# Kernel optimization log

Hardware: AMD Instinct MI355X
Metric: run time of the kernel (lower is better)

## Reference

```python
import jax, jax.numpy as jnp
import numpy as np

E = 8        # num experts
TOP = 2      # top-k
D = 1024     # emb_size


def setup_inputs() -> dict:
    key = jax.random.key(0)
    ks = jax.random.split(key, 8)
    s = 1.0 / np.sqrt(D)
    x = jax.random.normal(ks[0], (4, 2048, D), dtype=jnp.float32)
    Wg = jax.random.uniform(ks[1], (D, E), jnp.float32, -s, s)
    bg = jax.random.uniform(ks[2], (E,), jnp.float32, -s, s)
    W1 = jax.random.uniform(ks[3], (E, D, D), jnp.float32, -s, s)
    b1 = jax.random.uniform(ks[4], (E, D), jnp.float32, -s, s)
    W2 = jax.random.uniform(ks[5], (E, D, D), jnp.float32, -s, s)
    b2 = jax.random.uniform(ks[6], (E, D), jnp.float32, -s, s)
    return {"x": x, "Wg": Wg, "bg": bg, "W1": W1, "b1": b1, "W2": W2, "b2": b2}


def reference(x, Wg, bg, W1, b1, W2, b2):
    x_shape = x.shape
    xt = x.reshape(-1, x_shape[-1])                       # [N, D] tokens
    gate_prob = jax.nn.softmax(xt @ Wg + bg, axis=-1)     # [N, E]
    top_w, top_i = jax.lax.top_k(gate_prob, TOP)          # [N, TOP]
    top_w = jax.nn.softmax(top_w, axis=-1)                # renormalize over top-k
    N = xt.shape[0]
    # combine weights scattered into dense [N, E] (each token has TOP nonzeros)
    comb = jnp.zeros((N, E), xt.dtype).at[jnp.arange(N)[:, None], top_i].add(top_w)
    # per-expert 2-layer MLP applied to all tokens; masked-out tokens get 0 combine weight
    h = jax.nn.relu(jnp.einsum('nd,edf->enf', xt, W1) + b1[:, None, :])   # [E, N, D]
    ye = jnp.einsum('enf,efg->eng', h, W2) + b2[:, None, :]               # [E, N, D]
    y = jnp.einsum('ne,eng->ng', comb, ye)                                # [N, D]
    return y.reshape(x_shape), gate_prob
```

## Files before the change

### kernel.cpp

```cpp
#include <hip/hip_runtime.h>
#include <stdint.h>

#define TOKENS 8192
#define DIM    1024
#define NEXP   8
#define NASSIGN (TOKENS*2)
#define BK     64

#define C_ROW   16
#define C_TILE  25
#define C_TOTAL 34

#define WS_CTRL  0
#define WS_TOPE  1024
#define WS_TOPW  (WS_TOPE + NASSIGN*4)
#define WS_PTOK  (WS_TOPW + NASSIGN*4)
#define WS_PW    (WS_PTOK + NASSIGN*4)
#define WS_XB    (WS_PW  + NASSIGN*4)
#define WS_W1T   (WS_XB  + (size_t)TOKENS*DIM*2)
#define WS_W2T   (WS_W1T + (size_t)NEXP*DIM*DIM*2)
#define WS_H     (WS_W2T + (size_t)NEXP*DIM*DIM*2)

#define WGLD (DIM + 4)

typedef __attribute__((ext_vector_type(8))) short short8;
typedef __attribute__((ext_vector_type(4))) float floatx4;

__device__ __forceinline__ uint32_t bfr(float f) {
  uint32_t v = __float_as_uint(f);
  return (v + 0x7FFFu + ((v >> 16) & 1u)) >> 16;
}
__device__ __forceinline__ float b2f(uint32_t u) { return __uint_as_float(u << 16); }

__device__ __forceinline__ void load_lds16(const void* g, void* l) {
  __builtin_amdgcn_global_load_lds(
      (const __attribute__((address_space(1))) uint32_t*)g,
      (__attribute__((address_space(3))) uint32_t*)l, 16, 0, 0);
}

__global__ __launch_bounds__(256) void gate_kernel(
    const float* __restrict__ x, const float* __restrict__ Wg,
    const float* __restrict__ bg, float* __restrict__ gate_out,
    int* __restrict__ top_e, float* __restrict__ top_w,
    uint16_t* __restrict__ xb, float* __restrict__ y) {
  __shared__ __align__(16) float wgs[NEXP * WGLD];
  int t = threadIdx.x;

  {
    float4 z = make_float4(0.f, 0.f, 0.f, 0.f);
    float4* yz = (float4*)(y + (size_t)blockIdx.x * 4 * DIM);
    #pragma unroll
    for (int i = 0; i < 4; i++) yz[i * 256 + t] = z;
  }

  #pragma unroll
  for (int k = 0; k < 32; k++) {
    int i = k * 256 + t;
    float v = Wg[i];
    wgs[(i & 7) * WGLD + (i >> 3)] = v;
  }
  __syncthreads();

  int wave = t >> 6, lane = t & 63;
  int tok = blockIdx.x * 4 + wave;
  const float4* xr = (const float4*)(x + (size_t)tok * DIM);
  uint2* xw = (uint2*)(xb + (size_t)tok * DIM);

  float4 acc[NEXP];
  #pragma unroll
  for (int e = 0; e < NEXP; e++) acc[e] = make_float4(0.f, 0.f, 0.f, 0.f);

  #pragma unroll
  for (int c = 0; c < 4; c++) {
    float4 xv = xr[c * 64 + lane];
    uint2 o;
    o.x = bfr(xv.x) | (bfr(xv.y) << 16);
    o.y = bfr(xv.z) | (bfr(xv.w) << 16);
    xw[c * 64 + lane] = o;
    int d0 = (c * 64 + lane) * 4;
    #pragma unroll
    for (int e = 0; e < NEXP; e++) {
      float4 wv = *(const float4*)&wgs[e * WGLD + d0];
      acc[e].x = fmaf(xv.x, wv.x, acc[e].x);
      acc[e].y = fmaf(xv.y, wv.y, acc[e].y);
      acc[e].z = fmaf(xv.z, wv.z, acc[e].z);
      acc[e].w = fmaf(xv.w, wv.w, acc[e].w);
    }
  }
  float s[NEXP];
  #pragma unroll
  for (int e = 0; e < NEXP; e++) s[e] = (acc[e].x + acc[e].y) + (acc[e].z + acc[e].w);
  #pragma unroll
  for (int off = 32; off > 0; off >>= 1) {
    #pragma unroll
    for (int e = 0; e < NEXP; e++) s[e] += __shfl_xor(s[e], off);
  }
  if (lane == 0) {
    float lg[NEXP], p[NEXP];
    float mx = -1e30f;
    #pragma unroll
    for (int e = 0; e < NEXP; e++) { lg[e] = s[e] + bg[e]; mx = fmaxf(mx, lg[e]); }
    float sum = 0.f;
    #pragma unroll
    for (int e = 0; e < NEXP; e++) { p[e] = expf(lg[e] - mx); sum += p[e]; }
    float inv = 1.f / sum;
    #pragma unroll
    for (int e = 0; e < NEXP; e++) p[e] *= inv;
    float4* go = (float4*)(gate_out + (size_t)tok * NEXP);
    go[0] = make_float4(p[0], p[1], p[2], p[3]);
    go[1] = make_float4(p[4], p[5], p[6], p[7]);
    int i1 = 0;
    #pragma unroll
    for (int e = 1; e < NEXP; e++) if (p[e] > p[i1]) i1 = e;
    int i2 = (i1 == 0) ? 1 : 0;
    #pragma unroll
    for (int e = 0; e < NEXP; e++) if (e != i1 && p[e] > p[i2]) i2 = e;
    float ev = expf(p[i2] - p[i1]);
    float w1 = 1.f / (1.f + ev), w2 = ev / (1.f + ev);
    top_e[2*tok]   = i1; top_e[2*tok+1] = i2;
    top_w[2*tok]   = w1; top_w[2*tok+1] = w2;
  }
}

__global__ __launch_bounds__(256) void prep2_kernel(
    const float* __restrict__ W1, const float* __restrict__ W2,
    uint16_t* __restrict__ W1T, uint16_t* __restrict__ W2T,
    const int* __restrict__ top_e, const float* __restrict__ top_w,
    int* __restrict__ ctrl, int* __restrict__ ptok, float* __restrict__ pw) {
  __shared__ __align__(16) char smem[64 * 68 * 2];
  __shared__ int scnt[NEXP];
  __shared__ int rowstart[NEXP];
  int t = threadIdx.x;

  if (blockIdx.x != 0) {
    uint16_t (*tile)[68] = (uint16_t (*)[68])smem;
    int cb = blockIdx.x - 1;
    int m  = cb >> 8;
    int d0 = ((cb >> 4) & 15) * 64, f0 = (cb & 15) * 64;
    const float* src = (m < 8) ? (W1 + (size_t)m*DIM*DIM) : (W2 + (size_t)(m-8)*DIM*DIM);
    uint16_t*    dst = (m < 8) ? (W1T + (size_t)m*DIM*DIM) : (W2T + (size_t)(m-8)*DIM*DIM);
    int col = t & 63, rb = (t >> 6) * 16;
    #pragma unroll
    for (int i = 0; i < 16; i++) {
      int dr = rb + i;
      tile[dr][col] = (uint16_t)bfr(src[(size_t)(d0+dr)*DIM + f0 + col]);
    }
    __syncthreads();
    int dg = t & 15, frb = t >> 4;
    #pragma unroll
    for (int i = 0; i < 4; i++) {
      int fr = frb + i * 16;
      uint32_t b0 = tile[dg*4+0][fr], b1 = tile[dg*4+1][fr];
      uint32_t b2 = tile[dg*4+2][fr], b3 = tile[dg*4+3][fr];
      uint2 v;
      v.x = b0 | (b1 << 16);
      v.y = b2 | (b3 << 16);
      *(uint2*)&dst[(size_t)(f0+fr)*DIM + d0 + dg*4] = v;
    }
    return;
  }

  int* sc = (int*)smem;
  int cnt[NEXP];
  #pragma unroll
  for (int e = 0; e < NEXP; e++) cnt[e] = 0;
  for (int j = 0; j < 64; j++) {
    int e = top_e[t * 64 + j];
    cnt[e]++;
  }
  #pragma unroll
  for (int e = 0; e < NEXP; e++) sc[e * 256 + t] = cnt[e];
  __syncthreads();
  int wave = t >> 6, lane = t & 63;
  for (int ee = wave; ee < NEXP; ee += 4) {
    int running = 0;
    for (int chunk = 0; chunk < 4; chunk++) {
      int idx = ee * 256 + chunk * 64 + lane;
      int v = sc[idx];
      int incl = v;
      #pragma unroll
      for (int off = 1; off < 64; off <<= 1) {
        int u = __shfl_up(incl, off);
        if (lane >= off) incl += u;
      }
      sc[idx] = running + incl - v;
      running += __shfl(incl, 63);
    }
    if (lane == 0) scnt[ee] = running;
  }
  __syncthreads();
  if (t == 0) {
    int rs = 0, ts = 0;
    for (int e = 0; e < NEXP; e++) {
      ctrl[C_ROW + e] = rs;
      ctrl[C_TILE + e] = ts;
      rowstart[e] = rs;
      int c = scnt[e];
      rs += c;
      ts += (c + 127) >> 7;
    }
    ctrl[C_ROW + NEXP] = rs;
    ctrl[C_TILE + NEXP] = ts;
    ctrl[C_TOTAL] = ts;
  }
  __syncthreads();
  int off[NEXP];
  #pragma unroll
  for (int e = 0; e < NEXP; e++) off[e] = rowstart[e] + sc[e * 256 + t];
  for (int j = 0; j < 64; j++) {
    int i = t * 64 + j;
    int e = top_e[i];
    int pos = off[e]++;
    ptok[pos] = i >> 1;
    pw[pos]   = top_w[i];
  }
}

__device__ __forceinline__ bool sched_map(const int* ctrl, int bid,
                                          int& mtile, int& n0) {
  int total = ctrl[C_TOTAL];
  int spx = (total + 7) >> 3;
  int xcd = bid & 7, j = bid >> 3;
  int slot = j >> 3;
  if (slot >= spx) return false;
  mtile = xcd * spx + slot;
  n0 = (j & 7) * 128;
  return mtile < total;
}

__global__ __launch_bounds__(256, 2) void gemm1_kernel(
    const uint16_t* __restrict__ xb, const uint16_t* __restrict__ w1t,
    const float* __restrict__ b1, const int* __restrict__ ctrl,
    const int* __restrict__ ptok, uint16_t* __restrict__ h) {
  __shared__ __align__(16) uint16_t As[128*BK];
  __shared__ __align__(16) uint16_t Bs[128*BK];
  int mtile, n0;
  if (!sched_map(ctrl, blockIdx.x, mtile, n0)) return;
  int e = 0;
  #pragma unroll
  for (int k = 1; k < NEXP; k++) if (mtile >= ctrl[C_TILE + k]) e = k;
  int row0 = ctrl[C_ROW + e] + (mtile - ctrl[C_TILE + e]) * 128;
  int rend = ctrl[C_ROW + e + 1];

  int t = threadIdx.x, lane = t & 63, w = t >> 6;
  const uint16_t* gA[4];
  const uint16_t* gB[4];
  #pragma unroll
  for (int i = 0; i < 4; i++) {
    int s = i * 256 + t;
    int row = s >> 3, cs = s & 7;
    int gc = cs ^ (row & 7);
    int ar = row0 + row; if (ar > NASSIGN-1) ar = NASSIGN-1;
    int tok = ptok[ar];
    gA[i] = xb  + (size_t)tok * DIM + gc*8;
    gB[i] = w1t + (size_t)e*DIM*DIM + (size_t)(n0 + row)*DIM + gc*8;
  }
  floatx4 acc[4][4];
  #pragma unroll
  for (int mi = 0; mi < 4; mi++)
    #pragma unroll
    for (int ni = 0; ni < 4; ni++) acc[mi][ni] = (floatx4)(0.f);

  int wm = w & 1, wn = w >> 1;
  int l15 = lane & 15, lq = lane >> 4;

  for (int kt = 0; kt < DIM/BK; kt++) {
    #pragma unroll
    for (int i = 0; i < 4; i++) {
      load_lds16(gA[i], &As[(i*256 + t) * 8]);
      load_lds16(gB[i], &Bs[(i*256 + t) * 8]);
      gA[i] += BK; gB[i] += BK;
    }
    __syncthreads();
    #pragma unroll
    for (int ks = 0; ks < 2; ks++) {
      short8 a[4], b[4];
      #pragma unroll
      for (int mi = 0; mi < 4; mi++) {
        int row = wm*64 + mi*16 + l15;
        int slot = (ks*4 + lq) ^ (row & 7);
        a[mi] = *(const short8*)&As[row*BK + slot*8];
      }
      #pragma unroll
      for (int ni = 0; ni < 4; ni++) {
        int row = wn*64 + ni*16 + l15;
        int slot = (ks*4 + lq) ^ (row & 7);
        b[ni] = *(const short8*)&Bs[row*BK + slot*8];
      }
      #pragma unroll
      for (int mi = 0; mi < 4; mi++)
        #pragma unroll
        for (int ni = 0; ni < 4; ni++)
          acc[mi][ni] = __builtin_amdgcn_mfma_f32_16x16x32_bf16(a[mi], b[ni], acc[mi][ni], 0, 0, 0);
    }
    __syncthreads();
  }
  #pragma unroll
  for (int mi = 0; mi < 4; mi++) {
    #pragma unroll
    for (int r = 0; r < 4; r++) {
      int rt = wm*64 + mi*16 + lq*4 + r;
      int ar = row0 + rt;
      if (ar < rend) {
        #pragma unroll
        for (int ni = 0; ni < 4; ni++) {
          int n = n0 + wn*64 + ni*16 + l15;
          float v = acc[mi][ni][r] + b1[e*DIM + n];
          v = fmaxf(v, 0.f);
          h[(size_t)ar*DIM + n] = (uint16_t)bfr(v);
        }
      }
    }
  }
}

__global__ __launch_bounds__(256, 2) void gemm2_kernel(
    const uint16_t* __restrict__ h, const uint16_t* __restrict__ w2t,
    const float* __restrict__ b2, const int* __restrict__ ctrl,
    const int* __restrict__ ptok, const float* __restrict__ pw,
    float* __restrict__ y) {
  __shared__ __align__(16) uint16_t As[128*BK];
  __shared__ __align__(16) uint16_t Bs[128*BK];
  int mtile, n0;
  if (!sched_map(ctrl, blockIdx.x, mtile, n0)) return;
  int e = 0;
  #pragma unroll
  for (int k = 1; k < NEXP; k++) if (mtile >= ctrl[C_TILE + k]) e = k;
  int row0 = ctrl[C_ROW + e] + (mtile - ctrl[C_TILE + e]) * 128;
  int rend = ctrl[C_ROW + e + 1];

  int t = threadIdx.x, lane = t & 63, w = t >> 6;
  const uint16_t* gA[4];
  const uint16_t* gB[4];
  #pragma unroll
  for (int i = 0; i < 4; i++) {
    int s = i * 256 + t;
    int row = s >> 3, cs = s & 7;
    int gc = cs ^ (row & 7);
    int ar = row0 + row; if (ar > NASSIGN-1) ar = NASSIGN-1;
    gA[i] = h   + (size_t)ar * DIM + gc*8;
    gB[i] = w2t + (size_t)e*DIM*DIM + (size_t)(n0 + row)*DIM + gc*8;
  }
  floatx4 acc[4][4];
  #pragma unroll
  for (int mi = 0; mi < 4; mi++)
    #pragma unroll
    for (int ni = 0; ni < 4; ni++) acc[mi][ni] = (floatx4)(0.f);

  int wm = w & 1, wn = w >> 1;
  int l15 = lane & 15, lq = lane >> 4;

  for (int kt = 0; kt < DIM/BK; kt++) {
    #pragma unroll
    for (int i = 0; i < 4; i++) {
      load_lds16(gA[i], &As[(i*256 + t) * 8]);
      load_lds16(gB[i], &Bs[(i*256 + t) * 8]);
      gA[i] += BK; gB[i] += BK;
    }
    __syncthreads();
    #pragma unroll
    for (int ks = 0; ks < 2; ks++) {
      short8 a[4], b[4];
      #pragma unroll
      for (int mi = 0; mi < 4; mi++) {
        int row = wm*64 + mi*16 + l15;
        int slot = (ks*4 + lq) ^ (row & 7);
        a[mi] = *(const short8*)&As[row*BK + slot*8];
      }
      #pragma unroll
      for (int ni = 0; ni < 4; ni++) {
        int row = wn*64 + ni*16 + l15;
        int slot = (ks*4 + lq) ^ (row & 7);
        b[ni] = *(const short8*)&Bs[row*BK + slot*8];
      }
      #pragma unroll
      for (int mi = 0; mi < 4; mi++)
        #pragma unroll
        for (int ni = 0; ni < 4; ni++)
          acc[mi][ni] = __builtin_amdgcn_mfma_f32_16x16x32_bf16(a[mi], b[ni], acc[mi][ni], 0, 0, 0);
    }
    __syncthreads();
  }
  #pragma unroll
  for (int mi = 0; mi < 4; mi++) {
    #pragma unroll
    for (int r = 0; r < 4; r++) {
      int rt = wm*64 + mi*16 + lq*4 + r;
      int ar = row0 + rt;
      if (ar < rend) {
        int tok   = ptok[ar];
        float wgt = pw[ar];
        float* yrow = y + (size_t)tok * DIM;
        #pragma unroll
        for (int ni = 0; ni < 4; ni++) {
          int n = n0 + wn*64 + ni*16 + l15;
          float v = acc[mi][ni][r] + b2[e*DIM + n];
          unsafeAtomicAdd(&yrow[n], wgt * v);
        }
      }
    }
  }
}

extern "C" void kernel_launch(void* const* d_in, const int* in_sizes, int n_in,
                              void* d_out, int out_size, void* d_ws, size_t ws_size,
                              hipStream_t stream) {
  const float* x  = (const float*)d_in[0];
  const float* Wg = (const float*)d_in[1];
  const float* bg = (const float*)d_in[2];
  const float* W1 = (const float*)d_in[3];
  const float* b1 = (const float*)d_in[4];
  const float* W2 = (const float*)d_in[5];
  const float* b2 = (const float*)d_in[6];
  float* out = (float*)d_out;
  char* ws = (char*)d_ws;

  int*      ctrl = (int*)(ws + WS_CTRL);
  int*      tope = (int*)(ws + WS_TOPE);
  float*    topw = (float*)(ws + WS_TOPW);
  int*      ptok = (int*)(ws + WS_PTOK);
  float*    pww  = (float*)(ws + WS_PW);
  uint16_t* xb   = (uint16_t*)(ws + WS_XB);
  uint16_t* w1t  = (uint16_t*)(ws + WS_W1T);
  uint16_t* w2t  = (uint16_t*)(ws + WS_W2T);
  uint16_t* hbuf = (uint16_t*)(ws + WS_H);

  gate_kernel<<<2048, 256, 0, stream>>>(x, Wg, bg, out + (size_t)TOKENS*DIM,
                                        tope, topw, xb, out);
  prep2_kernel<<<4097, 256, 0, stream>>>(W1, W2, w1t, w2t, tope, topw,
                                         ctrl, ptok, pww);
  gemm1_kernel<<<136*8, 256, 0, stream>>>(xb, w1t, b1, ctrl, ptok, hbuf);
  gemm2_kernel<<<136*8, 256, 0, stream>>>(hbuf, w2t, b2, ctrl, ptok, pww, out);
}
```

Measured before the change: 329.7 us.

## Replace atomic scatter-add in gemm2 with bf16 per-assignment output and combine kernel

gemm2 no longer does fp32 atomic adds into y. It writes each assignment's expert output as bf16 into a buffer that reuses the xb workspace, and a new combine kernel gathers each token's two rows and sums them with the top-k weights. This also removes the zero-fill of y from the gate kernel and the pw permutation, adding an arow inverse map instead. The goal is to avoid scattered atomic traffic, at the cost of an extra kernel launch, an extra bf16 round trip through memory, and reduced precision in the expert outputs before combining.

```diff
diff --git a/kernel.cpp b/kernel.cpp
--- a/kernel.cpp
+++ b/kernel.cpp
@@ -15,11 +15,12 @@
 #define WS_TOPE  1024
 #define WS_TOPW  (WS_TOPE + NASSIGN*4)
 #define WS_PTOK  (WS_TOPW + NASSIGN*4)
-#define WS_PW    (WS_PTOK + NASSIGN*4)
-#define WS_XB    (WS_PW  + NASSIGN*4)
+#define WS_AROW  (WS_PTOK + NASSIGN*4)
+#define WS_XB    (WS_AROW + NASSIGN*4)
 #define WS_W1T   (WS_XB  + (size_t)TOKENS*DIM*2)
 #define WS_W2T   (WS_W1T + (size_t)NEXP*DIM*DIM*2)
 #define WS_H     (WS_W2T + (size_t)NEXP*DIM*DIM*2)
+#define WS_YE    WS_XB
 
 #define WGLD (DIM + 4)
 
@@ -42,16 +43,9 @@
     const float* __restrict__ x, const float* __restrict__ Wg,
     const float* __restrict__ bg, float* __restrict__ gate_out,
     int* __restrict__ top_e, float* __restrict__ top_w,
-    uint16_t* __restrict__ xb, float* __restrict__ y) {
+    uint16_t* __restrict__ xb) {
   __shared__ __align__(16) float wgs[NEXP * WGLD];
   int t = threadIdx.x;
-
-  {
-    float4 z = make_float4(0.f, 0.f, 0.f, 0.f);
-    float4* yz = (float4*)(y + (size_t)blockIdx.x * 4 * DIM);
-    #pragma unroll
-    for (int i = 0; i < 4; i++) yz[i * 256 + t] = z;
-  }
 
   #pragma unroll
   for (int k = 0; k < 32; k++) {
@@ -125,8 +119,8 @@
 __global__ __launch_bounds__(256) void prep2_kernel(
     const float* __restrict__ W1, const float* __restrict__ W2,
     uint16_t* __restrict__ W1T, uint16_t* __restrict__ W2T,
-    const int* __restrict__ top_e, const float* __restrict__ top_w,
-    int* __restrict__ ctrl, int* __restrict__ ptok, float* __restrict__ pw) {
+    const int* __restrict__ top_e,
+    int* __restrict__ ctrl, int* __restrict__ ptok, int* __restrict__ arow) {
   __shared__ __align__(16) char smem[64 * 68 * 2];
   __shared__ int scnt[NEXP];
   __shared__ int rowstart[NEXP];
@@ -212,7 +206,7 @@
     int e = top_e[i];
     int pos = off[e]++;
     ptok[pos] = i >> 1;
-    pw[pos]   = top_w[i];
+    arow[i] = pos;
   }
 }
 
@@ -317,8 +311,7 @@
 __global__ __launch_bounds__(256, 2) void gemm2_kernel(
     const uint16_t* __restrict__ h, const uint16_t* __restrict__ w2t,
     const float* __restrict__ b2, const int* __restrict__ ctrl,
-    const int* __restrict__ ptok, const float* __restrict__ pw,
-    float* __restrict__ y) {
+    uint16_t* __restrict__ yeb) {
   __shared__ __align__(16) uint16_t As[128*BK];
   __shared__ __align__(16) uint16_t Bs[128*BK];
   int mtile, n0;
@@ -388,18 +381,40 @@
       int rt = wm*64 + mi*16 + lq*4 + r;
       int ar = row0 + rt;
       if (ar < rend) {
-        int tok   = ptok[ar];
-        float wgt = pw[ar];
-        float* yrow = y + (size_t)tok * DIM;
         #pragma unroll
         for (int ni = 0; ni < 4; ni++) {
           int n = n0 + wn*64 + ni*16 + l15;
           float v = acc[mi][ni][r] + b2[e*DIM + n];
-          unsafeAtomicAdd(&yrow[n], wgt * v);
+          yeb[(size_t)ar*DIM + n] = (uint16_t)bfr(v);
         }
       }
     }
   }
+}
+
+__global__ __launch_bounds__(256) void combine_kernel(
+    const uint16_t* __restrict__ yeb, const int* __restrict__ arow,
+    const float* __restrict__ top_w, float* __restrict__ y) {
+  int t = threadIdx.x;
+  int tok = blockIdx.x * 2 + (t >> 7);
+  int i = t & 127;
+  int r0 = arow[2*tok], r1 = arow[2*tok+1];
+  float w0 = top_w[2*tok], w1 = top_w[2*tok+1];
+  const uint4* a = (const uint4*)(yeb + (size_t)r0 * DIM);
+  const uint4* b = (const uint4*)(yeb + (size_t)r1 * DIM);
+  uint4 av = a[i], bv = b[i];
+  float4* yo = (float4*)(y + (size_t)tok * DIM + i * 8);
+  float4 o0, o1;
+  o0.x = w0 * b2f(av.x & 0xFFFFu) + w1 * b2f(bv.x & 0xFFFFu);
+  o0.y = w0 * b2f(av.x >> 16)     + w1 * b2f(bv.x >> 16);
+  o0.z = w0 * b2f(av.y & 0xFFFFu) + w1 * b2f(bv.y & 0xFFFFu);
+  o0.w = w0 * b2f(av.y >> 16)     + w1 * b2f(bv.y >> 16);
+  o1.x = w0 * b2f(av.z & 0xFFFFu) + w1 * b2f(bv.z & 0xFFFFu);
+  o1.y = w0 * b2f(av.z >> 16)     + w1 * b2f(bv.z >> 16);
+  o1.z = w0 * b2f(av.w & 0xFFFFu) + w1 * b2f(bv.w & 0xFFFFu);
+  o1.w = w0 * b2f(av.w >> 16)     + w1 * b2f(bv.w >> 16);
+  yo[0] = o0;
+  yo[1] = o1;
 }
 
 extern "C" void kernel_launch(void* const* d_in, const int* in_sizes, int n_in,
@@ -419,16 +434,17 @@
   int*      tope = (int*)(ws + WS_TOPE);
   float*    topw = (float*)(ws + WS_TOPW);
   int*      ptok = (int*)(ws + WS_PTOK);
-  float*    pww  = (float*)(ws + WS_PW);
+  int*      arow = (int*)(ws + WS_AROW);
   uint16_t* xb   = (uint16_t*)(ws + WS_XB);
   uint16_t* w1t  = (uint16_t*)(ws + WS_W1T);
   uint16_t* w2t  = (uint16_t*)(ws + WS_W2T);
   uint16_t* hbuf = (uint16_t*)(ws + WS_H);
+  uint16_t* yeb  = (uint16_t*)(ws + WS_YE);
 
   gate_kernel<<<2048, 256, 0, stream>>>(x, Wg, bg, out + (size_t)TOKENS*DIM,
-                                        tope, topw, xb, out);
-  prep2_kernel<<<4097, 256, 0, stream>>>(W1, W2, w1t, w2t, tope, topw,
-                                         ctrl, ptok, pww);
+                                        tope, topw, xb);
+  prep2_kernel<<<4097, 256, 0, stream>>>(W1, W2, w1t, w2t, tope, ctrl, ptok, arow);
   gemm1_kernel<<<136*8, 256, 0, stream>>>(xb, w1t, b1, ctrl, ptok, hbuf);
-  gemm2_kernel<<<136*8, 256, 0, stream>>>(hbuf, w2t, b2, ctrl, ptok, pww, out);
-}
+  gemm2_kernel<<<136*8, 256, 0, stream>>>(hbuf, w2t, b2, ctrl, yeb);
+  combine_kernel<<<TOKENS/2, 256, 0, stream>>>(yeb, arow, topw, out);
+}
```

After: 281.9 us. -14.5%, faster.
